# Kernel optimization log

Measured on AMD Instinct MI355X. Metric: run time of the kernel, lower is better.

The kernel has to match this reference:

```python
import jax, jax.numpy as jnp
import numpy as np

MUL = 128            # multiplicity of 0e and 1o node irreps
N_NODES = 10000
N_EDGES = 160000
R_BASIS = 8          # edge_feats_irreps.num_irreps
HIDDEN = 64
W_NUMEL = 4 * MUL    # conv_tp.weight_numel (4 uvu paths, edge mul = 1)
SQRT3 = 3.0 ** 0.5
SILU_2MOM = 1.679177   # e3nn normalize2mom constant for SiLU
AVG_NUM_NEIGHBORS = 10.0


def setup_inputs() -> dict:
    key = jax.random.key(0)
    ks = jax.random.split(key, 12)
    rn = lambda k, s: jax.random.normal(k, s, dtype=jnp.float32)
    return {
        "node_feats": rn(ks[0], (N_NODES, 4 * MUL)),        # 128x0e + 128x1o
        "edge_attrs": rn(ks[1], (N_EDGES, 4)),               # 1x0e + 1x1o spherical harmonics
        "edge_feats": rn(ks[2], (N_EDGES, R_BASIS)),         # 8x0e radial basis
        "edge_index": jax.random.randint(ks[3], (2, N_EDGES), 0, N_NODES),
        "W_up0": rn(ks[4], (MUL, MUL)),                      # linear_up, 0e block
        "W_up1": rn(ks[5], (MUL, MUL)),                      # linear_up, 1o block
        "W_mlp1": rn(ks[6], (R_BASIS, HIDDEN)),
        "W_mlp2": rn(ks[7], (HIDDEN, HIDDEN)),
        "W_mlp3": rn(ks[8], (HIDDEN, HIDDEN)),
        "W_mlp4": rn(ks[9], (HIDDEN, W_NUMEL)),
        "W_out0": rn(ks[10], (2 * MUL, MUL)),                # linear: 256x0e -> 128x0e
        "W_out1": rn(ks[11], (2 * MUL, MUL)),                # linear: 256x1o -> 128x1o
    }


def _lin_irreps(x0, x1, W0, W1):
    # equivariant o3.Linear: per-irrep channel mixing with 1/sqrt(fan_in)
    y0 = (x0 @ W0) / jnp.sqrt(jnp.float32(W0.shape[0]))
    y1 = jnp.einsum('num,uv->nvm', x1, W1) / jnp.sqrt(jnp.float32(W1.shape[0]))
    return y0, y1


def _forward(node_feats, edge_attrs, edge_feats, edge_index,
             W_up0, W_up1, W_mlp1, W_mlp2, W_mlp3, W_mlp4, W_out0, W_out1):
    num_nodes = node_feats.shape[0]
    sender, receiver = edge_index[0], edge_index[1]

    # split node feats into irrep blocks: [N,128] scalars, [N,128,3] vectors
    x0 = node_feats[:, :MUL]
    x1 = node_feats[:, MUL:].reshape(num_nodes, MUL, 3)
    x0, x1 = _lin_irreps(x0, x1, W_up0, W_up1)  # linear_up

    # radial MLP (e3nn FullyConnectedNet with normalized SiLU) -> per-edge TP weights
    h = edge_feats
    for W in (W_mlp1, W_mlp2, W_mlp3):
        h = SILU_2MOM * jax.nn.silu((h @ W) / jnp.sqrt(jnp.float32(W.shape[0])))
    tpw = (h @ W_mlp4) / jnp.sqrt(jnp.float32(W_mlp4.shape[0]))  # [E, 4*MUL]
    w1, w2, w3, w4 = jnp.split(tpw, 4, axis=-1)  # per-path [E, MUL]

    # gather sender features
    s0 = x0[sender]              # [E, MUL]
    s1 = x1[sender]              # [E, MUL, 3]
    y0 = edge_attrs[:, 0:1]      # [E, 1]  (0e sh)
    y1 = edge_attrs[:, 1:4]      # [E, 3]  (1o sh)

    # weighted uvu CG tensor product (component norm: alpha = sqrt(2l_out+1), w3j sum-sq = 1)
    p1 = w1 * s0 * y0                                    # 0e x 0e -> 0e  [E, MUL]
    p2 = (w2 * s0)[:, :, None] * y1[:, None, :]          # 0e x 1o -> 1o  [E, MUL, 3]
    p3 = w3[:, :, None] * s1 * y0[:, None, :]            # 1o x 0e -> 1o  [E, MUL, 3]
    p4 = w4 * jnp.einsum('eum,em->eu', s1, y1) / SQRT3   # 1o x 1o -> 0e  [E, MUL]

    # irreps_mid.simplify() = 256x0e + 256x1o
    m0 = jnp.concatenate([p1, p4], axis=-1)              # [E, 2*MUL]
    m1 = jnp.concatenate([p2, p3], axis=1)               # [E, 2*MUL, 3]

    # scatter-sum over receivers
    msg0 = jax.ops.segment_sum(m0, receiver, num_segments=num_nodes)
    msg1 = jax.ops.segment_sum(m1, receiver, num_segments=num_nodes)

    o0, o1 = _lin_irreps(msg0, msg1, W_out0, W_out1)
    out = jnp.concatenate([o0, o1.reshape(num_nodes, 3 * MUL)], axis=-1)
    return out / AVG_NUM_NEIGHBORS


def reference(node_feats, edge_attrs, edge_feats, edge_index,
              W_up0, W_up1, W_mlp1, W_mlp2, W_mlp3, W_mlp4, W_out0, W_out1):
    return _forward(node_feats, edge_attrs, edge_feats, edge_index,
                    W_up0, W_up1, W_mlp1, W_mlp2, W_mlp3, W_mlp4, W_out0, W_out1)
```

## Files before the change

kernel.cpp:

```cpp
#include <hip/hip_runtime.h>
#include <stdint.h>

#define NN 10000
#define NE 160000

typedef short short8 __attribute__((ext_vector_type(8)));
typedef float f32x4 __attribute__((ext_vector_type(4)));

__device__ __forceinline__ float bf2f(unsigned short u) {
    return __uint_as_float(((uint32_t)u) << 16);
}
__device__ __forceinline__ float bflo(uint32_t u) { return __uint_as_float(u << 16); }
__device__ __forceinline__ float bfhi(uint32_t u) { return __uint_as_float(u & 0xffff0000u); }
__device__ __forceinline__ unsigned short f2bf(float f) {
    uint32_t u = __float_as_uint(f);
    u += 0x7fffu + ((u >> 16) & 1u);
    return (unsigned short)(u >> 16);
}
__device__ __forceinline__ uint32_t pack2(float lo, float hi) {
    return (uint32_t)f2bf(lo) | ((uint32_t)f2bf(hi) << 16);
}
__device__ __forceinline__ float silu2(float x) {
    return 1.679177f * x / (1.f + __expf(-x));
}

__global__ __launch_bounds__(256) void k_wup(const float* __restrict__ Wu0,
                                             const float* __restrict__ Wu1,
                                             unsigned short* __restrict__ w0T,
                                             unsigned short* __restrict__ w1T) {
    const float s = 0.08838834764831845f;
    for (int i = threadIdx.x + blockIdx.x * 256; i < 16384; i += 256 * 64) {
        int u = i >> 7, v = i & 127;
        w0T[v * 128 + u] = f2bf(Wu0[i] * s);
        w1T[v * 128 + u] = f2bf(Wu1[i] * s);
    }
}

__global__ __launch_bounds__(256) void k_prep(const float* __restrict__ nf,
                                              unsigned short* __restrict__ x0b,
                                              unsigned short* __restrict__ x1b) {
    int idx = blockIdx.x * 256 + threadIdx.x;
    int n = idx >> 7, u = idx & 127;
    const float* row = nf + (size_t)n * 512;
    x0b[(size_t)n * 128 + u] = f2bf(row[u]);
    const float* p = row + 128 + u * 3;
    x1b[(size_t)n * 128 + u]                = f2bf(p[0]);
    x1b[1280000 + (size_t)n * 128 + u]      = f2bf(p[1]);
    x1b[2560000 + (size_t)n * 128 + u]      = f2bf(p[2]);
}

__global__ __launch_bounds__(256) void k_upg(const unsigned short* __restrict__ x0b,
                                             const unsigned short* __restrict__ x1b,
                                             const unsigned short* __restrict__ w0T,
                                             const unsigned short* __restrict__ w1T,
                                             float* __restrict__ xw) {
    int wave = threadIdx.x >> 6, lane = threadIdx.x & 63;
    int wid = blockIdx.x * 4 + wave;
    if (wid >= 1250) return;
    int tile = wid >> 1, half = wid & 1;
    int n0 = tile * 16;
    int lm = lane & 15, lq = lane >> 4;

    uint4 A0[4], A1[3][4];
    const unsigned short* a0r = x0b + (size_t)(n0 + lm) * 128 + lq * 8;
#pragma unroll
    for (int kf = 0; kf < 4; ++kf) A0[kf] = *(const uint4*)(a0r + kf * 32);
#pragma unroll
    for (int m = 0; m < 3; ++m) {
        const unsigned short* a1r = x1b + 1280000 * (size_t)m + (size_t)(n0 + lm) * 128 + lq * 8;
#pragma unroll
        for (int kf = 0; kf < 4; ++kf) A1[m][kf] = *(const uint4*)(a1r + kf * 32);
    }

    for (int vq = 0; vq < 4; ++vq) {
        int vt = half * 4 + vq;
        const unsigned short* b0r = w0T + (vt * 16 + lm) * 128 + lq * 8;
        const unsigned short* b1r = w1T + (vt * 16 + lm) * 128 + lq * 8;
        f32x4 acc0 = {0.f, 0.f, 0.f, 0.f};
#pragma unroll
        for (int kf = 0; kf < 4; ++kf) {
            short8 b = __builtin_bit_cast(short8, *(const uint4*)(b0r + kf * 32));
            acc0 = __builtin_amdgcn_mfma_f32_16x16x32_bf16(
                __builtin_bit_cast(short8, A0[kf]), b, acc0, 0, 0, 0);
        }
        f32x4 acc1[3];
#pragma unroll
        for (int m = 0; m < 3; ++m) acc1[m] = (f32x4){0.f, 0.f, 0.f, 0.f};
#pragma unroll
        for (int kf = 0; kf < 4; ++kf) {
            short8 b = __builtin_bit_cast(short8, *(const uint4*)(b1r + kf * 32));
#pragma unroll
            for (int m = 0; m < 3; ++m)
                acc1[m] = __builtin_amdgcn_mfma_f32_16x16x32_bf16(
                    __builtin_bit_cast(short8, A1[m][kf]), b, acc1[m], 0, 0, 0);
        }
        int col = vt * 16 + lm;
#pragma unroll
        for (int r = 0; r < 4; ++r) {
            float* o = xw + (size_t)(n0 + lq * 4 + r) * 512;
            o[col] = acc0[r];
            o[128 + col] = acc1[0][r];
            o[256 + col] = acc1[1][r];
            o[384 + col] = acc1[2][r];
        }
    }
}

__global__ __launch_bounds__(256) void k_wmlp(const float* __restrict__ W1,
                                              const float* __restrict__ W2,
                                              const float* __restrict__ W3,
                                              unsigned short* __restrict__ w1Tp,
                                              unsigned short* __restrict__ w2T,
                                              unsigned short* __restrict__ w3T) {
    int t = threadIdx.x;
    for (int i = t; i < 2048; i += 256) {
        int jj = i >> 5, k = i & 31;
        w1Tp[i] = (k < 8) ? f2bf(W1[k * 64 + jj] * 0.3535533905932738f) : 0;
    }
    for (int i = t; i < 4096; i += 256) {
        int jj = i >> 6, k = i & 63;
        w2T[i] = f2bf(W2[k * 64 + jj] * 0.125f);
        w3T[i] = f2bf(W3[k * 64 + jj] * 0.125f);
    }
}

__global__ __launch_bounds__(256) void k_mlp(const float* __restrict__ ef,
                                             const unsigned short* __restrict__ w1Tp,
                                             const unsigned short* __restrict__ w2T,
                                             const unsigned short* __restrict__ w3T,
                                             unsigned short* __restrict__ h3w) {
    __shared__ __align__(16) unsigned short hs_all[4][64 * 72];
    int wave = threadIdx.x >> 6, lane = threadIdx.x & 63;
    int lm = lane & 15, lq = lane >> 4;
    int e0 = blockIdx.x * 256 + wave * 64;
    unsigned short* h = hs_all[wave];

    uint4 A1[4];
#pragma unroll
    for (int mt = 0; mt < 4; ++mt)
        A1[mt] = *(const uint4*)(w1Tp + (mt * 16 + lm) * 32 + lq * 8);
#pragma unroll
    for (int nt = 0; nt < 4; ++nt) {
        uint4 b = {0, 0, 0, 0};
        if (lq == 0) {
            const float4* p = (const float4*)(ef + (size_t)(e0 + nt * 16 + lm) * 8);
            float4 x = p[0], y = p[1];
            b.x = pack2(x.x, x.y); b.y = pack2(x.z, x.w);
            b.z = pack2(y.x, y.y); b.w = pack2(y.z, y.w);
        }
        short8 bb = __builtin_bit_cast(short8, b);
        unsigned short* hrow = h + (nt * 16 + lm) * 72;
#pragma unroll
        for (int mt = 0; mt < 4; ++mt) {
            f32x4 acc = {0.f, 0.f, 0.f, 0.f};
            acc = __builtin_amdgcn_mfma_f32_16x16x32_bf16(
                __builtin_bit_cast(short8, A1[mt]), bb, acc, 0, 0, 0);
            uint2 v;
            v.x = pack2(silu2(acc[0]), silu2(acc[1]));
            v.y = pack2(silu2(acc[2]), silu2(acc[3]));
            *(uint2*)(hrow + mt * 16 + lq * 4) = v;
        }
    }

    uint4 A2[4][2];
#pragma unroll
    for (int mt = 0; mt < 4; ++mt)
#pragma unroll
        for (int kf = 0; kf < 2; ++kf)
            A2[mt][kf] = *(const uint4*)(w2T + (mt * 16 + lm) * 64 + kf * 32 + lq * 8);
#pragma unroll
    for (int nt = 0; nt < 4; ++nt) {
        unsigned short* hrow = h + (nt * 16 + lm) * 72;
        short8 B0 = __builtin_bit_cast(short8, *(const uint4*)(hrow + lq * 8));
        short8 B1 = __builtin_bit_cast(short8, *(const uint4*)(hrow + 32 + lq * 8));
#pragma unroll
        for (int mt = 0; mt < 4; ++mt) {
            f32x4 acc = {0.f, 0.f, 0.f, 0.f};
            acc = __builtin_amdgcn_mfma_f32_16x16x32_bf16(
                __builtin_bit_cast(short8, A2[mt][0]), B0, acc, 0, 0, 0);
            acc = __builtin_amdgcn_mfma_f32_16x16x32_bf16(
                __builtin_bit_cast(short8, A2[mt][1]), B1, acc, 0, 0, 0);
            uint2 v;
            v.x = pack2(silu2(acc[0]), silu2(acc[1]));
            v.y = pack2(silu2(acc[2]), silu2(acc[3]));
            *(uint2*)(hrow + mt * 16 + lq * 4) = v;
        }
    }

    uint4 A3[4][2];
#pragma unroll
    for (int mt = 0; mt < 4; ++mt)
#pragma unroll
        for (int kf = 0; kf < 2; ++kf)
            A3[mt][kf] = *(const uint4*)(w3T + (mt * 16 + lm) * 64 + kf * 32 + lq * 8);
#pragma unroll
    for (int nt = 0; nt < 4; ++nt) {
        unsigned short* hrow = h + (nt * 16 + lm) * 72;
        short8 B0 = __builtin_bit_cast(short8, *(const uint4*)(hrow + lq * 8));
        short8 B1 = __builtin_bit_cast(short8, *(const uint4*)(hrow + 32 + lq * 8));
#pragma unroll
        for (int mt = 0; mt < 4; ++mt) {
            f32x4 acc = {0.f, 0.f, 0.f, 0.f};
            acc = __builtin_amdgcn_mfma_f32_16x16x32_bf16(
                __builtin_bit_cast(short8, A3[mt][0]), B0, acc, 0, 0, 0);
            acc = __builtin_amdgcn_mfma_f32_16x16x32_bf16(
                __builtin_bit_cast(short8, A3[mt][1]), B1, acc, 0, 0, 0);
            uint2 v;
            v.x = pack2(silu2(acc[0]), silu2(acc[1]));
            v.y = pack2(silu2(acc[2]), silu2(acc[3]));
            *(uint2*)(hrow + mt * 16 + lq * 4) = v;
        }
    }

    const unsigned short* hr = h + lane * 72;
    uint4* og = (uint4*)(h3w + (size_t)(e0 + lane) * 64);
#pragma unroll
    for (int q = 0; q < 8; ++q) og[q] = *(const uint4*)(hr + q * 8);
}

__global__ void k_zero(int* __restrict__ p, int n) {
    int i = blockIdx.x * 256 + threadIdx.x;
    if (i < n) p[i] = 0;
}
__global__ void k_hist(const int* __restrict__ ei, int* __restrict__ counts) {
    int e = blockIdx.x * 256 + threadIdx.x;
    if (e < NE) atomicAdd(&counts[ei[NE + e]], 1);
}
__global__ __launch_bounds__(1024) void k_scan(const int* __restrict__ counts,
                                               int* __restrict__ offs,
                                               int* __restrict__ cursor) {
    __shared__ int sums[1024];
    int t = threadIdx.x;
    int base = t * 10;
    int s = 0;
    for (int i = 0; i < 10; ++i) {
        int idx = base + i;
        if (idx < NN) s += counts[idx];
    }
    sums[t] = s;
    __syncthreads();
    for (int d = 1; d < 1024; d <<= 1) {
        int v = (t >= d) ? sums[t - d] : 0;
        __syncthreads();
        if (t >= d) sums[t] += v;
        __syncthreads();
    }
    int run = (t == 0) ? 0 : sums[t - 1];
    for (int i = 0; i < 10; ++i) {
        int idx = base + i;
        if (idx < NN) {
            offs[idx] = run;
            cursor[idx] = run;
            run += counts[idx];
        }
    }
    if (t == 0) offs[NN] = NE;
}
__global__ void k_fill(const int* __restrict__ ei, int* __restrict__ cursor,
                       int* __restrict__ elist) {
    int e = blockIdx.x * 256 + threadIdx.x;
    if (e < NE) {
        int slot = atomicAdd(&cursor[ei[NE + e]], 1);
        elist[slot] = e;
    }
}
__global__ void k_gather(const int* __restrict__ ei, const float* __restrict__ ea,
                         const int* __restrict__ elist,
                         int* __restrict__ eis, float4* __restrict__ eap) {
    int i = blockIdx.x * 256 + threadIdx.x;
    if (i < NE) {
        int e = elist[i];
        eis[i] = ei[e];
        eap[i] = *(const float4*)(ea + (size_t)e * 4);
    }
}

__global__ void k_w4t(const float* __restrict__ W4, unsigned short* __restrict__ w4T) {
    int idx = blockIdx.x * 256 + threadIdx.x;
    int k = idx >> 9, c = idx & 511;
    w4T[c * 64 + k] = f2bf(W4[idx]);
}
__global__ void k_wt2(const float* __restrict__ Wo0, const float* __restrict__ Wo1,
                      unsigned short* __restrict__ woT0, unsigned short* __restrict__ woT1) {
    int idx = blockIdx.x * 256 + threadIdx.x;
    int u = idx >> 7, v = idx & 127;
    woT0[v * 256 + u] = f2bf(Wo0[idx]);
    woT1[v * 256 + u] = f2bf(Wo1[idx]);
}

__global__ __launch_bounds__(256) void k_tpw(const unsigned short* __restrict__ h3w,
                                             const unsigned short* __restrict__ w4T,
                                             const int* __restrict__ elist,
                                             unsigned short* __restrict__ tpw) {
    int wave = threadIdx.x >> 6, lane = threadIdx.x & 63;
    int e0 = blockIdx.x * 256 + wave * 64;
    int lm = lane & 15, lq = lane >> 4;
    uint4 B[4][2];
#pragma unroll
    for (int n = 0; n < 4; ++n) {
        int esrc = elist[e0 + n * 16 + lm];
#pragma unroll
        for (int k = 0; k < 2; ++k)
            B[n][k] = *(const uint4*)(h3w + (size_t)esrc * 64 + k * 32 + lq * 8);
    }
    const unsigned short* aw = w4T + lm * 64 + lq * 8;
    unsigned short* op = tpw + (size_t)e0 * 512;
#pragma unroll 2
    for (int m = 0; m < 32; ++m) {
        f32x4 acc0 = {0.f, 0.f, 0.f, 0.f};
        f32x4 acc1 = {0.f, 0.f, 0.f, 0.f};
        f32x4 acc2 = {0.f, 0.f, 0.f, 0.f};
        f32x4 acc3 = {0.f, 0.f, 0.f, 0.f};
#pragma unroll
        for (int k = 0; k < 2; ++k) {
            uint4 a_raw = *(const uint4*)(aw + m * 1024 + k * 32);
            short8 a = __builtin_bit_cast(short8, a_raw);
            acc0 = __builtin_amdgcn_mfma_f32_16x16x32_bf16(a, __builtin_bit_cast(short8, B[0][k]), acc0, 0, 0, 0);
            acc1 = __builtin_amdgcn_mfma_f32_16x16x32_bf16(a, __builtin_bit_cast(short8, B[1][k]), acc1, 0, 0, 0);
            acc2 = __builtin_amdgcn_mfma_f32_16x16x32_bf16(a, __builtin_bit_cast(short8, B[2][k]), acc2, 0, 0, 0);
            acc3 = __builtin_amdgcn_mfma_f32_16x16x32_bf16(a, __builtin_bit_cast(short8, B[3][k]), acc3, 0, 0, 0);
        }
        int cb = m * 16 + lq * 4;
        uint2 v;
        v.x = pack2(acc0[0] * 0.125f, acc0[1] * 0.125f);
        v.y = pack2(acc0[2] * 0.125f, acc0[3] * 0.125f);
        *(uint2*)(op + (size_t)(0 * 16 + lm) * 512 + cb) = v;
        v.x = pack2(acc1[0] * 0.125f, acc1[1] * 0.125f);
        v.y = pack2(acc1[2] * 0.125f, acc1[3] * 0.125f);
        *(uint2*)(op + (size_t)(1 * 16 + lm) * 512 + cb) = v;
        v.x = pack2(acc2[0] * 0.125f, acc2[1] * 0.125f);
        v.y = pack2(acc2[2] * 0.125f, acc2[3] * 0.125f);
        *(uint2*)(op + (size_t)(2 * 16 + lm) * 512 + cb) = v;
        v.x = pack2(acc3[0] * 0.125f, acc3[1] * 0.125f);
        v.y = pack2(acc3[2] * 0.125f, acc3[3] * 0.125f);
        *(uint2*)(op + (size_t)(3 * 16 + lm) * 512 + cb) = v;
    }
}

__global__ __launch_bounds__(256) void k_msg2(const float* __restrict__ xw,
                                              const unsigned short* __restrict__ tpw,
                                              const int* __restrict__ eis,
                                              const float4* __restrict__ eap,
                                              const int* __restrict__ offs,
                                              unsigned short* __restrict__ msgb) {
    int n = blockIdx.x, t = threadIdx.x;
    int j = t >> 6, c0 = (t & 63) * 2;
    int beg = offs[n], end = offs[n + 1];
    float a0 = 0.f, a1 = 0.f, a2 = 0.f, a3 = 0.f, a4 = 0.f, a5 = 0.f;
    for (int i = beg; i < end; ++i) {
        int snd = eis[i];
        float4 eav = eap[i];
        float y0 = eav.x, y1x = eav.y, y1y = eav.z, y1z = eav.w;
        uint32_t wp = ((const uint32_t*)tpw)[(size_t)i * 256 + t];
        float wa = bflo(wp), wb = bfhi(wp);
        const float* xr = xw + (size_t)snd * 512;
        if (j == 0) {
            a0 += wa * xr[c0] * y0;
            a1 += wb * xr[c0 + 1] * y0;
        } else if (j == 1) {
            float ta = wa * xr[c0], tb = wb * xr[c0 + 1];
            a0 += ta * y1x; a1 += ta * y1y; a2 += ta * y1z;
            a3 += tb * y1x; a4 += tb * y1y; a5 += tb * y1z;
        } else if (j == 2) {
            float f0 = wa * y0, f1 = wb * y0;
            a0 += f0 * xr[128 + c0]; a1 += f0 * xr[256 + c0]; a2 += f0 * xr[384 + c0];
            a3 += f1 * xr[128 + c0 + 1]; a4 += f1 * xr[256 + c0 + 1]; a5 += f1 * xr[384 + c0 + 1];
        } else {
            float dta = xr[128 + c0] * y1x + xr[256 + c0] * y1y + xr[384 + c0] * y1z;
            float dtb = xr[128 + c0 + 1] * y1x + xr[256 + c0 + 1] * y1y + xr[384 + c0 + 1] * y1z;
            a0 += wa * dta * 0.5773502691896258f;
            a1 += wb * dtb * 0.5773502691896258f;
        }
    }
    unsigned short* mr = msgb + (size_t)n * 1024;
    if (j == 0) {
        *(uint32_t*)(mr + c0) = pack2(a0, a1);
    } else if (j == 1) {
        *(uint32_t*)(mr + 256 + c0)       = pack2(a0, a3);
        *(uint32_t*)(mr + 256 + 256 + c0) = pack2(a1, a4);
        *(uint32_t*)(mr + 256 + 512 + c0) = pack2(a2, a5);
    } else if (j == 2) {
        *(uint32_t*)(mr + 256 + 128 + c0)       = pack2(a0, a3);
        *(uint32_t*)(mr + 256 + 256 + 128 + c0) = pack2(a1, a4);
        *(uint32_t*)(mr + 256 + 512 + 128 + c0) = pack2(a2, a5);
    } else {
        *(uint32_t*)(mr + 128 + c0) = pack2(a0, a1);
    }
}

__global__ __launch_bounds__(256) void k_out0(const unsigned short* __restrict__ msgb,
                                              const unsigned short* __restrict__ woT,
                                              float* __restrict__ out) {
    int wave = threadIdx.x >> 6, lane = threadIdx.x & 63;
    int wid = blockIdx.x * 4 + wave;
    if (wid >= NN / 16) return;
    int n0 = wid * 16;
    int lm = lane & 15, lq = lane >> 4;
    uint4 A[8];
    const unsigned short* ar = msgb + (size_t)(n0 + lm) * 1024 + lq * 8;
#pragma unroll
    for (int kf = 0; kf < 8; ++kf) A[kf] = *(const uint4*)(ar + kf * 32);
    const unsigned short* br = woT + lm * 256 + lq * 8;
    float* ob = out + (size_t)n0 * 512;
    for (int vt = 0; vt < 8; ++vt) {
        f32x4 acc = {0.f, 0.f, 0.f, 0.f};
#pragma unroll
        for (int kf = 0; kf < 8; ++kf) {
            uint4 b = *(const uint4*)(br + vt * 16 * 256 + kf * 32);
            acc = __builtin_amdgcn_mfma_f32_16x16x32_bf16(
                __builtin_bit_cast(short8, A[kf]), __builtin_bit_cast(short8, b), acc, 0, 0, 0);
        }
#pragma unroll
        for (int r = 0; r < 4; ++r)
            ob[(size_t)(lq * 4 + r) * 512 + vt * 16 + lm] = acc[r] * 0.00625f;
    }
}

__global__ __launch_bounds__(256) void k_out1(const unsigned short* __restrict__ msgb,
                                              const unsigned short* __restrict__ woT,
                                              float* __restrict__ out) {
    int wave = threadIdx.x >> 6, lane = threadIdx.x & 63;
    int wid = blockIdx.x * 4 + wave;
    if (wid >= NN / 16) return;
    int n0 = wid * 16;
    int lm = lane & 15, lq = lane >> 4;
    uint4 A[3][8];
    const unsigned short* ar = msgb + (size_t)(n0 + lm) * 1024 + 256 + lq * 8;
#pragma unroll
    for (int m = 0; m < 3; ++m)
#pragma unroll
        for (int kf = 0; kf < 8; ++kf)
            A[m][kf] = *(const uint4*)(ar + m * 256 + kf * 32);
    const unsigned short* br = woT + lm * 256 + lq * 8;
    float* ob = out + (size_t)n0 * 512 + 128;
    for (int vt = 0; vt < 8; ++vt) {
        f32x4 acc[3];
#pragma unroll
        for (int m = 0; m < 3; ++m) acc[m] = (f32x4){0.f, 0.f, 0.f, 0.f};
#pragma unroll
        for (int kf = 0; kf < 8; ++kf) {
            uint4 braw = *(const uint4*)(br + vt * 16 * 256 + kf * 32);
            short8 b = __builtin_bit_cast(short8, braw);
#pragma unroll
            for (int m = 0; m < 3; ++m)
                acc[m] = __builtin_amdgcn_mfma_f32_16x16x32_bf16(
                    __builtin_bit_cast(short8, A[m][kf]), b, acc[m], 0, 0, 0);
        }
        int vb = (vt * 16 + lm) * 3;
#pragma unroll
        for (int r = 0; r < 4; ++r) {
            float* o = ob + (size_t)(lq * 4 + r) * 512 + vb;
            o[0] = acc[0][r] * 0.00625f;
            o[1] = acc[1][r] * 0.00625f;
            o[2] = acc[2][r] * 0.00625f;
        }
    }
}

extern "C" void kernel_launch(void* const* d_in, const int* in_sizes, int n_in,
                              void* d_out, int out_size, void* d_ws, size_t ws_size,
                              hipStream_t stream) {
    const float* nf  = (const float*)d_in[0];
    const float* ea  = (const float*)d_in[1];
    const float* ef  = (const float*)d_in[2];
    const int*   ei  = (const int*)d_in[3];
    const float* Wu0 = (const float*)d_in[4];
    const float* Wu1 = (const float*)d_in[5];
    const float* W1  = (const float*)d_in[6];
    const float* W2  = (const float*)d_in[7];
    const float* W3  = (const float*)d_in[8];
    const float* W4  = (const float*)d_in[9];
    const float* Wo0 = (const float*)d_in[10];
    const float* Wo1 = (const float*)d_in[11];
    float* out = (float*)d_out;
    char* ws = (char*)d_ws;

    unsigned short* tpw  = (unsigned short*)ws;
    unsigned short* x0b  = (unsigned short*)ws;
    unsigned short* x1b  = (unsigned short*)(ws + 2560000);
    float*          xw   = (float*)(ws + 163840000);
    unsigned short* h3w  = (unsigned short*)(ws + 184320000);
    unsigned short* woT0 = (unsigned short*)(ws + 184320000);
    unsigned short* woT1 = (unsigned short*)(ws + 184320000 + 65536);
    float4*         eap  = (float4*)(ws + 184320000 + 131072);
    int*            eis  = (int*)(ws + 184320000 + 131072 + 2560000);
    unsigned short* msgb = (unsigned short*)(ws + 204800000);
    unsigned short* w4T  = (unsigned short*)(ws + 225280000);
    int* ib     = (int*)(ws + 225280000 + 65536);
    int* counts = ib;
    int* offs   = ib + 10240;
    int* cursor = ib + 20480;
    int* elist  = ib + 30720;
    unsigned short* w1Tp = (unsigned short*)(ws + 226108416);
    unsigned short* w2T  = (unsigned short*)(ws + 226108416 + 4096);
    unsigned short* w3T  = (unsigned short*)(ws + 226108416 + 12288);
    unsigned short* w0T  = (unsigned short*)(ws + 226128896);
    unsigned short* w1T  = (unsigned short*)(ws + 226161664);

    k_wmlp <<<1, 256, 0, stream>>>(W1, W2, W3, w1Tp, w2T, w3T);
    k_wup  <<<64, 256, 0, stream>>>(Wu0, Wu1, w0T, w1T);
    k_prep <<<5000, 256, 0, stream>>>(nf, x0b, x1b);
    k_upg  <<<313, 256, 0, stream>>>(x0b, x1b, w0T, w1T, xw);
    k_mlp  <<<625, 256, 0, stream>>>(ef, w1Tp, w2T, w3T, h3w);
    k_w4t  <<<128, 256, 0, stream>>>(W4, w4T);
    k_zero <<<40, 256, 0, stream>>>(counts, NN);
    k_hist <<<625, 256, 0, stream>>>(ei, counts);
    k_scan <<<1, 1024, 0, stream>>>(counts, offs, cursor);
    k_fill <<<625, 256, 0, stream>>>(ei, cursor, elist);
    k_tpw  <<<625, 256, 0, stream>>>(h3w, w4T, elist, tpw);
    k_wt2  <<<128, 256, 0, stream>>>(Wo0, Wo1, woT0, woT1);
    k_gather<<<625, 256, 0, stream>>>(ei, ea, elist, eis, eap);
    k_msg2 <<<NN, 256, 0, stream>>>(xw, tpw, eis, eap, offs, msgb);
    k_out0 <<<157, 256, 0, stream>>>(msgb, woT0, out);
    k_out1 <<<157, 256, 0, stream>>>(msgb, woT1, out);
}
```

Before: 385.6 us.

## Fuse TP weight GEMM into message aggregation via LDS tiles and segmented atomics

Merges the per-edge tensor-product weight GEMM and the receiver-sorted message aggregation into one kernel. Each block computes weights for its 256 edges in 64-edge chunks and stages them in shared memory, then accumulates per receiver. A receiver segment that crosses a block boundary is flushed with fp32 atomics into a zeroed buffer. This removes the large bf16 per-edge weight buffer round-trip through global memory. In exchange it adds a memset, an fp32 message buffer, far fewer blocks, and atomic contention. The 1/8 scale is folded into W4 on conversion.

```diff
diff --git a/kernel.cpp b/kernel.cpp
--- a/kernel.cpp
+++ b/kernel.cpp
@@ -257,11 +257,13 @@
     if (t == 0) offs[NN] = NE;
 }
 __global__ void k_fill(const int* __restrict__ ei, int* __restrict__ cursor,
-                       int* __restrict__ elist) {
+                       int* __restrict__ elist, int* __restrict__ rix) {
     int e = blockIdx.x * 256 + threadIdx.x;
     if (e < NE) {
-        int slot = atomicAdd(&cursor[ei[NE + e]], 1);
+        int r = ei[NE + e];
+        int slot = atomicAdd(&cursor[r], 1);
         elist[slot] = e;
+        rix[slot] = r;
     }
 }
 __global__ void k_gather(const int* __restrict__ ei, const float* __restrict__ ea,
@@ -278,7 +280,7 @@
 __global__ void k_w4t(const float* __restrict__ W4, unsigned short* __restrict__ w4T) {
     int idx = blockIdx.x * 256 + threadIdx.x;
     int k = idx >> 9, c = idx & 511;
-    w4T[c * 64 + k] = f2bf(W4[idx]);
+    w4T[c * 64 + k] = f2bf(W4[idx] * 0.125f);
 }
 __global__ void k_wt2(const float* __restrict__ Wo0, const float* __restrict__ Wo1,
                       unsigned short* __restrict__ woT0, unsigned short* __restrict__ woT1) {
@@ -288,107 +290,134 @@
     woT1[v * 256 + u] = f2bf(Wo1[idx]);
 }
 
-__global__ __launch_bounds__(256) void k_tpw(const unsigned short* __restrict__ h3w,
-                                             const unsigned short* __restrict__ w4T,
-                                             const int* __restrict__ elist,
-                                             unsigned short* __restrict__ tpw) {
-    int wave = threadIdx.x >> 6, lane = threadIdx.x & 63;
-    int e0 = blockIdx.x * 256 + wave * 64;
+__global__ __launch_bounds__(256) void k_tpmsg(const unsigned short* __restrict__ h3w,
+                                               const unsigned short* __restrict__ w4T,
+                                               const int* __restrict__ elist,
+                                               const int* __restrict__ eis,
+                                               const int* __restrict__ rix,
+                                               const float4* __restrict__ eap,
+                                               const int* __restrict__ offs,
+                                               const float* __restrict__ xw,
+                                               float* __restrict__ msg) {
+    __shared__ __align__(16) unsigned short tile[64 * 520];
+    int t = threadIdx.x;
+    int wave = t >> 6, lane = t & 63;
     int lm = lane & 15, lq = lane >> 4;
-    uint4 B[4][2];
-#pragma unroll
-    for (int n = 0; n < 4; ++n) {
-        int esrc = elist[e0 + n * 16 + lm];
-#pragma unroll
-        for (int k = 0; k < 2; ++k)
-            B[n][k] = *(const uint4*)(h3w + (size_t)esrc * 64 + k * 32 + lq * 8);
-    }
+    int blockStart = blockIdx.x * 256;
+    int blockEnd = blockStart + 256;
+    int j = t >> 6;
+    int c0 = (t & 63) * 2;
+
     const unsigned short* aw = w4T + lm * 64 + lq * 8;
-    unsigned short* op = tpw + (size_t)e0 * 512;
-#pragma unroll 2
-    for (int m = 0; m < 32; ++m) {
-        f32x4 acc0 = {0.f, 0.f, 0.f, 0.f};
-        f32x4 acc1 = {0.f, 0.f, 0.f, 0.f};
-        f32x4 acc2 = {0.f, 0.f, 0.f, 0.f};
-        f32x4 acc3 = {0.f, 0.f, 0.f, 0.f};
-#pragma unroll
-        for (int k = 0; k < 2; ++k) {
-            uint4 a_raw = *(const uint4*)(aw + m * 1024 + k * 32);
-            short8 a = __builtin_bit_cast(short8, a_raw);
-            acc0 = __builtin_amdgcn_mfma_f32_16x16x32_bf16(a, __builtin_bit_cast(short8, B[0][k]), acc0, 0, 0, 0);
-            acc1 = __builtin_amdgcn_mfma_f32_16x16x32_bf16(a, __builtin_bit_cast(short8, B[1][k]), acc1, 0, 0, 0);
-            acc2 = __builtin_amdgcn_mfma_f32_16x16x32_bf16(a, __builtin_bit_cast(short8, B[2][k]), acc2, 0, 0, 0);
-            acc3 = __builtin_amdgcn_mfma_f32_16x16x32_bf16(a, __builtin_bit_cast(short8, B[3][k]), acc3, 0, 0, 0);
-        }
-        int cb = m * 16 + lq * 4;
-        uint2 v;
-        v.x = pack2(acc0[0] * 0.125f, acc0[1] * 0.125f);
-        v.y = pack2(acc0[2] * 0.125f, acc0[3] * 0.125f);
-        *(uint2*)(op + (size_t)(0 * 16 + lm) * 512 + cb) = v;
-        v.x = pack2(acc1[0] * 0.125f, acc1[1] * 0.125f);
-        v.y = pack2(acc1[2] * 0.125f, acc1[3] * 0.125f);
-        *(uint2*)(op + (size_t)(1 * 16 + lm) * 512 + cb) = v;
-        v.x = pack2(acc2[0] * 0.125f, acc2[1] * 0.125f);
-        v.y = pack2(acc2[2] * 0.125f, acc2[3] * 0.125f);
-        *(uint2*)(op + (size_t)(2 * 16 + lm) * 512 + cb) = v;
-        v.x = pack2(acc3[0] * 0.125f, acc3[1] * 0.125f);
-        v.y = pack2(acc3[2] * 0.125f, acc3[3] * 0.125f);
-        *(uint2*)(op + (size_t)(3 * 16 + lm) * 512 + cb) = v;
-    }
-}
-
-__global__ __launch_bounds__(256) void k_msg2(const float* __restrict__ xw,
-                                              const unsigned short* __restrict__ tpw,
-                                              const int* __restrict__ eis,
-                                              const float4* __restrict__ eap,
-                                              const int* __restrict__ offs,
-                                              unsigned short* __restrict__ msgb) {
-    int n = blockIdx.x, t = threadIdx.x;
-    int j = t >> 6, c0 = (t & 63) * 2;
-    int beg = offs[n], end = offs[n + 1];
+
     float a0 = 0.f, a1 = 0.f, a2 = 0.f, a3 = 0.f, a4 = 0.f, a5 = 0.f;
-    for (int i = beg; i < end; ++i) {
-        int snd = eis[i];
-        float4 eav = eap[i];
-        float y0 = eav.x, y1x = eav.y, y1y = eav.z, y1z = eav.w;
-        uint32_t wp = ((const uint32_t*)tpw)[(size_t)i * 256 + t];
-        float wa = bflo(wp), wb = bfhi(wp);
-        const float* xr = xw + (size_t)snd * 512;
+    int curR = rix[blockStart];
+
+    auto doFlush = [&](int r) {
+        float* mr = msg + (size_t)r * 1024;
+        bool bnd = (offs[r] < blockStart) || (offs[r + 1] > blockEnd);
         if (j == 0) {
-            a0 += wa * xr[c0] * y0;
-            a1 += wb * xr[c0 + 1] * y0;
+            if (bnd) { atomicAdd(&mr[c0], a0); atomicAdd(&mr[c0 + 1], a1); }
+            else { mr[c0] = a0; mr[c0 + 1] = a1; }
         } else if (j == 1) {
-            float ta = wa * xr[c0], tb = wb * xr[c0 + 1];
-            a0 += ta * y1x; a1 += ta * y1y; a2 += ta * y1z;
-            a3 += tb * y1x; a4 += tb * y1y; a5 += tb * y1z;
+            if (bnd) {
+                atomicAdd(&mr[256 + c0], a0); atomicAdd(&mr[256 + c0 + 1], a3);
+                atomicAdd(&mr[512 + c0], a1); atomicAdd(&mr[512 + c0 + 1], a4);
+                atomicAdd(&mr[768 + c0], a2); atomicAdd(&mr[768 + c0 + 1], a5);
+            } else {
+                mr[256 + c0] = a0; mr[256 + c0 + 1] = a3;
+                mr[512 + c0] = a1; mr[512 + c0 + 1] = a4;
+                mr[768 + c0] = a2; mr[768 + c0 + 1] = a5;
+            }
         } else if (j == 2) {
-            float f0 = wa * y0, f1 = wb * y0;
-            a0 += f0 * xr[128 + c0]; a1 += f0 * xr[256 + c0]; a2 += f0 * xr[384 + c0];
-            a3 += f1 * xr[128 + c0 + 1]; a4 += f1 * xr[256 + c0 + 1]; a5 += f1 * xr[384 + c0 + 1];
+            if (bnd) {
+                atomicAdd(&mr[384 + c0], a0); atomicAdd(&mr[384 + c0 + 1], a3);
+                atomicAdd(&mr[640 + c0], a1); atomicAdd(&mr[640 + c0 + 1], a4);
+                atomicAdd(&mr[896 + c0], a2); atomicAdd(&mr[896 + c0 + 1], a5);
+            } else {
+                mr[384 + c0] = a0; mr[384 + c0 + 1] = a3;
+                mr[640 + c0] = a1; mr[640 + c0 + 1] = a4;
+                mr[896 + c0] = a2; mr[896 + c0 + 1] = a5;
+            }
         } else {
-            float dta = xr[128 + c0] * y1x + xr[256 + c0] * y1y + xr[384 + c0] * y1z;
-            float dtb = xr[128 + c0 + 1] * y1x + xr[256 + c0 + 1] * y1y + xr[384 + c0 + 1] * y1z;
-            a0 += wa * dta * 0.5773502691896258f;
-            a1 += wb * dtb * 0.5773502691896258f;
-        }
-    }
-    unsigned short* mr = msgb + (size_t)n * 1024;
-    if (j == 0) {
-        *(uint32_t*)(mr + c0) = pack2(a0, a1);
-    } else if (j == 1) {
-        *(uint32_t*)(mr + 256 + c0)       = pack2(a0, a3);
-        *(uint32_t*)(mr + 256 + 256 + c0) = pack2(a1, a4);
-        *(uint32_t*)(mr + 256 + 512 + c0) = pack2(a2, a5);
-    } else if (j == 2) {
-        *(uint32_t*)(mr + 256 + 128 + c0)       = pack2(a0, a3);
-        *(uint32_t*)(mr + 256 + 256 + 128 + c0) = pack2(a1, a4);
-        *(uint32_t*)(mr + 256 + 512 + 128 + c0) = pack2(a2, a5);
-    } else {
-        *(uint32_t*)(mr + 128 + c0) = pack2(a0, a1);
-    }
-}
-
-__global__ __launch_bounds__(256) void k_out0(const unsigned short* __restrict__ msgb,
+            if (bnd) { atomicAdd(&mr[128 + c0], a0); atomicAdd(&mr[128 + c0 + 1], a1); }
+            else { mr[128 + c0] = a0; mr[128 + c0 + 1] = a1; }
+        }
+        a0 = a1 = a2 = a3 = a4 = a5 = 0.f;
+    };
+
+    for (int chunk = 0; chunk < 4; ++chunk) {
+        int cbase = blockStart + chunk * 64;
+
+        uint4 B[4][2];
+#pragma unroll
+        for (int nt = 0; nt < 4; ++nt) {
+            int esrc = elist[cbase + nt * 16 + lm];
+            B[nt][0] = *(const uint4*)(h3w + (size_t)esrc * 64 + lq * 8);
+            B[nt][1] = *(const uint4*)(h3w + (size_t)esrc * 64 + 32 + lq * 8);
+        }
+#pragma unroll
+        for (int ml = 0; ml < 8; ++ml) {
+            int m = wave * 8 + ml;
+            f32x4 acc0 = {0.f, 0.f, 0.f, 0.f};
+            f32x4 acc1 = {0.f, 0.f, 0.f, 0.f};
+            f32x4 acc2 = {0.f, 0.f, 0.f, 0.f};
+            f32x4 acc3 = {0.f, 0.f, 0.f, 0.f};
+#pragma unroll
+            for (int k = 0; k < 2; ++k) {
+                short8 a = __builtin_bit_cast(short8, *(const uint4*)(aw + m * 1024 + k * 32));
+                acc0 = __builtin_amdgcn_mfma_f32_16x16x32_bf16(a, __builtin_bit_cast(short8, B[0][k]), acc0, 0, 0, 0);
+                acc1 = __builtin_amdgcn_mfma_f32_16x16x32_bf16(a, __builtin_bit_cast(short8, B[1][k]), acc1, 0, 0, 0);
+                acc2 = __builtin_amdgcn_mfma_f32_16x16x32_bf16(a, __builtin_bit_cast(short8, B[2][k]), acc2, 0, 0, 0);
+                acc3 = __builtin_amdgcn_mfma_f32_16x16x32_bf16(a, __builtin_bit_cast(short8, B[3][k]), acc3, 0, 0, 0);
+            }
+            int cb = m * 16 + lq * 4;
+            uint2 v;
+            v.x = pack2(acc0[0], acc0[1]); v.y = pack2(acc0[2], acc0[3]);
+            *(uint2*)(tile + (0 * 16 + lm) * 520 + cb) = v;
+            v.x = pack2(acc1[0], acc1[1]); v.y = pack2(acc1[2], acc1[3]);
+            *(uint2*)(tile + (1 * 16 + lm) * 520 + cb) = v;
+            v.x = pack2(acc2[0], acc2[1]); v.y = pack2(acc2[2], acc2[3]);
+            *(uint2*)(tile + (2 * 16 + lm) * 520 + cb) = v;
+            v.x = pack2(acc3[0], acc3[1]); v.y = pack2(acc3[2], acc3[3]);
+            *(uint2*)(tile + (3 * 16 + lm) * 520 + cb) = v;
+        }
+        __syncthreads();
+
+        for (int e = 0; e < 64; ++e) {
+            int slot = cbase + e;
+            int r = rix[slot];
+            if (r != curR) { doFlush(curR); curR = r; }
+            int snd = eis[slot];
+            float4 eav = eap[slot];
+            float y0 = eav.x, y1x = eav.y, y1y = eav.z, y1z = eav.w;
+            uint32_t wp = *(const uint32_t*)(tile + e * 520 + t * 2);
+            float wa = bflo(wp), wb = bfhi(wp);
+            const float* xr = xw + (size_t)snd * 512;
+            if (j == 0) {
+                a0 += wa * xr[c0] * y0;
+                a1 += wb * xr[c0 + 1] * y0;
+            } else if (j == 1) {
+                float ta = wa * xr[c0], tb = wb * xr[c0 + 1];
+                a0 += ta * y1x; a1 += ta * y1y; a2 += ta * y1z;
+                a3 += tb * y1x; a4 += tb * y1y; a5 += tb * y1z;
+            } else if (j == 2) {
+                float f0 = wa * y0, f1 = wb * y0;
+                a0 += f0 * xr[128 + c0]; a1 += f0 * xr[256 + c0]; a2 += f0 * xr[384 + c0];
+                a3 += f1 * xr[128 + c0 + 1]; a4 += f1 * xr[256 + c0 + 1]; a5 += f1 * xr[384 + c0 + 1];
+            } else {
+                float dta = xr[128 + c0] * y1x + xr[256 + c0] * y1y + xr[384 + c0] * y1z;
+                float dtb = xr[128 + c0 + 1] * y1x + xr[256 + c0 + 1] * y1y + xr[384 + c0 + 1] * y1z;
+                a0 += wa * dta * 0.5773502691896258f;
+                a1 += wb * dtb * 0.5773502691896258f;
+            }
+        }
+        __syncthreads();
+    }
+    doFlush(curR);
+}
+
+__global__ __launch_bounds__(256) void k_out0(const float* __restrict__ msg,
                                               const unsigned short* __restrict__ woT,
                                               float* __restrict__ out) {
     int wave = threadIdx.x >> 6, lane = threadIdx.x & 63;
@@ -397,9 +426,14 @@
     int n0 = wid * 16;
     int lm = lane & 15, lq = lane >> 4;
     uint4 A[8];
-    const unsigned short* ar = msgb + (size_t)(n0 + lm) * 1024 + lq * 8;
-#pragma unroll
-    for (int kf = 0; kf < 8; ++kf) A[kf] = *(const uint4*)(ar + kf * 32);
+    const float* ar = msg + (size_t)(n0 + lm) * 1024 + lq * 8;
+#pragma unroll
+    for (int kf = 0; kf < 8; ++kf) {
+        float4 f0 = *(const float4*)(ar + kf * 32);
+        float4 f1 = *(const float4*)(ar + kf * 32 + 4);
+        A[kf] = (uint4){pack2(f0.x, f0.y), pack2(f0.z, f0.w),
+                        pack2(f1.x, f1.y), pack2(f1.z, f1.w)};
+    }
     const unsigned short* br = woT + lm * 256 + lq * 8;
     float* ob = out + (size_t)n0 * 512;
     for (int vt = 0; vt < 8; ++vt) {
@@ -416,7 +450,7 @@
     }
 }
 
-__global__ __launch_bounds__(256) void k_out1(const unsigned short* __restrict__ msgb,
+__global__ __launch_bounds__(256) void k_out1(const float* __restrict__ msg,
                                               const unsigned short* __restrict__ woT,
                                               float* __restrict__ out) {
     int wave = threadIdx.x >> 6, lane = threadIdx.x & 63;
@@ -425,12 +459,16 @@
     int n0 = wid * 16;
     int lm = lane & 15, lq = lane >> 4;
     uint4 A[3][8];
-    const unsigned short* ar = msgb + (size_t)(n0 + lm) * 1024 + 256 + lq * 8;
+    const float* ar = msg + (size_t)(n0 + lm) * 1024 + 256 + lq * 8;
 #pragma unroll
     for (int m = 0; m < 3; ++m)
 #pragma unroll
-        for (int kf = 0; kf < 8; ++kf)
-            A[m][kf] = *(const uint4*)(ar + m * 256 + kf * 32);
+        for (int kf = 0; kf < 8; ++kf) {
+            float4 f0 = *(const float4*)(ar + m * 256 + kf * 32);
+            float4 f1 = *(const float4*)(ar + m * 256 + kf * 32 + 4);
+            A[m][kf] = (uint4){pack2(f0.x, f0.y), pack2(f0.z, f0.w),
+                               pack2(f1.x, f1.y), pack2(f1.z, f1.w)};
+        }
     const unsigned short* br = woT + lm * 256 + lq * 8;
     float* ob = out + (size_t)n0 * 512 + 128;
     for (int vt = 0; vt < 8; ++vt) {
@@ -475,27 +513,27 @@
     float* out = (float*)d_out;
     char* ws = (char*)d_ws;
 
-    unsigned short* tpw  = (unsigned short*)ws;
-    unsigned short* x0b  = (unsigned short*)ws;
-    unsigned short* x1b  = (unsigned short*)(ws + 2560000);
-    float*          xw   = (float*)(ws + 163840000);
-    unsigned short* h3w  = (unsigned short*)(ws + 184320000);
-    unsigned short* woT0 = (unsigned short*)(ws + 184320000);
-    unsigned short* woT1 = (unsigned short*)(ws + 184320000 + 65536);
-    float4*         eap  = (float4*)(ws + 184320000 + 131072);
-    int*            eis  = (int*)(ws + 184320000 + 131072 + 2560000);
-    unsigned short* msgb = (unsigned short*)(ws + 204800000);
-    unsigned short* w4T  = (unsigned short*)(ws + 225280000);
-    int* ib     = (int*)(ws + 225280000 + 65536);
+    float*          xw   = (float*)ws;
+    unsigned short* h3w  = (unsigned short*)(ws + 20480000);
+    float*          msg  = (float*)(ws + 40960000);
+    unsigned short* x0b  = (unsigned short*)(ws + 81920000);
+    unsigned short* x1b  = (unsigned short*)(ws + 84480000);
+    unsigned short* w4T  = (unsigned short*)(ws + 92160000);
+    unsigned short* woT0 = (unsigned short*)(ws + 92225536);
+    unsigned short* woT1 = (unsigned short*)(ws + 92291072);
+    float4*         eap  = (float4*)(ws + 92356608);
+    int* ib     = (int*)(ws + 94916608);
     int* counts = ib;
     int* offs   = ib + 10240;
     int* cursor = ib + 20480;
     int* elist  = ib + 30720;
-    unsigned short* w1Tp = (unsigned short*)(ws + 226108416);
-    unsigned short* w2T  = (unsigned short*)(ws + 226108416 + 4096);
-    unsigned short* w3T  = (unsigned short*)(ws + 226108416 + 12288);
-    unsigned short* w0T  = (unsigned short*)(ws + 226128896);
-    unsigned short* w1T  = (unsigned short*)(ws + 226161664);
+    int* rix    = ib + 190720;
+    int* eis    = ib + 350720;
+    unsigned short* w1Tp = (unsigned short*)(ws + 96959488);
+    unsigned short* w2T  = (unsigned short*)(ws + 96963584);
+    unsigned short* w3T  = (unsigned short*)(ws + 96971776);
+    unsigned short* w0T  = (unsigned short*)(ws + 96979968);
+    unsigned short* w1T  = (unsigned short*)(ws + 97012736);
 
     k_wmlp <<<1, 256, 0, stream>>>(W1, W2, W3, w1Tp, w2T, w3T);
     k_wup  <<<64, 256, 0, stream>>>(Wu0, Wu1, w0T, w1T);
@@ -503,14 +541,14 @@
     k_upg  <<<313, 256, 0, stream>>>(x0b, x1b, w0T, w1T, xw);
     k_mlp  <<<625, 256, 0, stream>>>(ef, w1Tp, w2T, w3T, h3w);
     k_w4t  <<<128, 256, 0, stream>>>(W4, w4T);
+    k_wt2  <<<128, 256, 0, stream>>>(Wo0, Wo1, woT0, woT1);
     k_zero <<<40, 256, 0, stream>>>(counts, NN);
     k_hist <<<625, 256, 0, stream>>>(ei, counts);
     k_scan <<<1, 1024, 0, stream>>>(counts, offs, cursor);
-    k_fill <<<625, 256, 0, stream>>>(ei, cursor, elist);
-    k_tpw  <<<625, 256, 0, stream>>>(h3w, w4T, elist, tpw);
-    k_wt2  <<<128, 256, 0, stream>>>(Wo0, Wo1, woT0, woT1);
+    k_fill <<<625, 256, 0, stream>>>(ei, cursor, elist, rix);
     k_gather<<<625, 256, 0, stream>>>(ei, ea, elist, eis, eap);
-    k_msg2 <<<NN, 256, 0, stream>>>(xw, tpw, eis, eap, offs, msgb);
-    k_out0 <<<157, 256, 0, stream>>>(msgb, woT0, out);
-    k_out1 <<<157, 256, 0, stream>>>(msgb, woT1, out);
-}
+    hipMemsetAsync(msg, 0, 40960000, stream);
+    k_tpmsg<<<625, 256, 0, stream>>>(h3w, w4T, elist, eis, rix, eap, offs, xw, msg);
+    k_out0 <<<157, 256, 0, stream>>>(msg, woT0, out);
+    k_out1 <<<157, 256, 0, stream>>>(msg, woT1, out);
+}
```

New measurement: 513.6 us. 1.33x slower.
